# Optimization experiments

Measured on AMD Instinct MI355X. Metric: run time of the kernel, lower is better.

The kernel has to match this reference:

```python
import jax, jax.numpy as jnp
import numpy as np

B, S, D, H = 2, 2048, 768, 12
DH = D // H


def setup_inputs() -> dict:
    key = jax.random.key(0)
    ks = jax.random.split(key, 12)
    f32 = jnp.float32
    sd = 1.0 / np.sqrt(D)
    return {
        "q": jax.random.normal(ks[0], (B, S, D), f32),
        "k": jax.random.normal(ks[1], (B, S, D), f32),
        "v": jax.random.normal(ks[2], (B, S, D), f32),
        "mask": jax.random.normal(ks[3], (S, S), f32),
        "Wq": jax.random.normal(ks[4], (D, D), f32) * sd,
        "bq": jnp.zeros((D,), f32),
        "Wk": jax.random.normal(ks[5], (D, D), f32) * sd,
        "bk": jnp.zeros((D,), f32),
        "Wv": jax.random.normal(ks[6], (D, D), f32) * sd,
        "bv": jnp.zeros((D,), f32),
        "Wo": jax.random.normal(ks[7], (D, D), f32) * sd,
        "bo": jnp.zeros((D,), f32),
    }


def reference(q, k, v, mask, Wq, bq, Wk, bk, Wv, bv, Wo, bo):
    # torch nn.Linear: y = x @ W.T + b
    qh = (q @ Wq.T + bq).reshape(B, S, H, DH).transpose(0, 2, 1, 3)  # [B,H,S,DH]
    kh = (k @ Wk.T + bk).reshape(B, S, H, DH).transpose(0, 2, 1, 3)
    vh = (v @ Wv.T + bv).reshape(B, S, H, DH).transpose(0, 2, 1, 3)
    scores = jnp.einsum("bhsd,bhtd->bhst", qh, kh)  # [B,H,S,S]
    # original adds mask after permute to [H,B,S,S]; with an [S,S] mask the
    # broadcast add is identical either way
    scores = scores + mask
    attn = jax.nn.softmax(scores.astype(jnp.float32) / np.sqrt(DH), axis=-1)
    out = jnp.einsum("bhst,bhtd->bhsd", attn, vh)  # [B,H,S,DH]
    out = out.transpose(0, 2, 1, 3).reshape(B, S, D)
    return out @ Wo.T + bo
```

## Files before the change

### kernel.cpp

```cpp
#include <hip/hip_runtime.h>
#include <hip/hip_bf16.h>

#define B_ 2
#define S_ 2048
#define D_ 768
#define H_ 12
#define DH_ 64
#define M_ (B_*S_)
#define BH_ (B_*H_)

typedef __bf16 v8bf __attribute__((ext_vector_type(8)));
typedef __bf16 v4bf __attribute__((ext_vector_type(4)));
typedef float  v4f  __attribute__((ext_vector_type(4)));

static __device__ __forceinline__ v4f mfma16(v8bf a, v8bf b, v4f c) {
  return __builtin_amdgcn_mfma_f32_16x16x32_bf16(a, b, c, 0, 0, 0);
}

static __device__ __forceinline__ void gload_lds16(const __bf16* g, __bf16* l) {
  __builtin_amdgcn_global_load_lds(
      (const __attribute__((address_space(1))) unsigned int*)g,
      (__attribute__((address_space(3))) unsigned int*)l,
      16, 0, 0);
}

#define C1_ 0.18033688011112042f

__global__ __launch_bounds__(256) void convert_kernel(
    const float* __restrict__ q, const float* __restrict__ k, const float* __restrict__ v,
    const float* __restrict__ Wq, const float* __restrict__ Wk,
    const float* __restrict__ Wv, const float* __restrict__ Wo,
    __bf16* __restrict__ Xq, __bf16* __restrict__ Xk, __bf16* __restrict__ Xv,
    __bf16* __restrict__ Wqb, __bf16* __restrict__ Wkb,
    __bf16* __restrict__ Wvb, __bf16* __restrict__ Wob)
{
  const float* src; __bf16* dst; int n;
  switch (blockIdx.y) {
    case 0: src = q;  dst = Xq;  n = M_*D_; break;
    case 1: src = k;  dst = Xk;  n = M_*D_; break;
    case 2: src = v;  dst = Xv;  n = M_*D_; break;
    case 3: src = Wq; dst = Wqb; n = D_*D_; break;
    case 4: src = Wk; dst = Wkb; n = D_*D_; break;
    case 5: src = Wv; dst = Wvb; n = D_*D_; break;
    default: src = Wo; dst = Wob; n = D_*D_; break;
  }
  int n4 = n >> 2;
  for (int i = blockIdx.x*blockDim.x + threadIdx.x; i < n4; i += gridDim.x*blockDim.x) {
    float4 x = ((const float4*)src)[i];
    v4bf y;
    y[0] = (__bf16)x.x; y[1] = (__bf16)x.y; y[2] = (__bf16)x.z; y[3] = (__bf16)x.w;
    ((v4bf*)dst)[i] = y;
  }
}

__global__ __launch_bounds__(256) void em_kernel(
    const float* __restrict__ mask, __bf16* __restrict__ em)
{
  int t = blockIdx.x*256 + threadIdx.x;
  int L = t & 63; int rest = t >> 6;
  int w = rest & 7; rest >>= 3;
  int kt = rest & 63; rest >>= 6;
  int qt = rest;
  int row = qt*128 + w*16 + (L & 15);
  int key0 = kt*32 + ((L >> 4) << 2);
  const float* mp = mask + (size_t)row*S_ + key0;
  float4 m0 = *(const float4*)mp;
  float4 m1 = *(const float4*)(mp + 16);
  v8bf e;
  e[0] = (__bf16)exp2f(C1_*m0.x); e[1] = (__bf16)exp2f(C1_*m0.y);
  e[2] = (__bf16)exp2f(C1_*m0.z); e[3] = (__bf16)exp2f(C1_*m0.w);
  e[4] = (__bf16)exp2f(C1_*m1.x); e[5] = (__bf16)exp2f(C1_*m1.y);
  e[6] = (__bf16)exp2f(C1_*m1.z); e[7] = (__bf16)exp2f(C1_*m1.w);
  *(v8bf*)(em + (size_t)t*8) = e;
}

static __device__ __forceinline__ void gemm128_pipe(
    const __bf16* __restrict__ A, const __bf16* __restrict__ W,
    int m0, int n0, __bf16* lds, v4f acc[4][4])
{
  const int lane = threadIdx.x & 63;
  const int wave = threadIdx.x >> 6;
  const int r16 = lane & 15;
  const int kc8 = (lane >> 4) << 3;
  const int ia = (wave >> 1) << 2;
  const int ib = (wave & 1) << 2;

  const __bf16* gsrc[4]; int ldo[4];
  #pragma unroll
  for (int t = 0; t < 4; t++) {
    int fb = wave*4 + t;
    gsrc[t] = (fb < 8)
        ? A + (size_t)(m0 + fb*16 + r16)*D_ + kc8
        : W + (size_t)(n0 + (fb - 8)*16 + r16)*D_ + kc8;
    ldo[t] = fb << 9;
  }

  asm volatile("" ::: "memory");
  #pragma unroll
  for (int t = 0; t < 4; t++) gload_lds16(gsrc[t], lds + ldo[t]);
  asm volatile("" ::: "memory");
  #pragma unroll
  for (int t = 0; t < 4; t++) gload_lds16(gsrc[t] + 32, lds + 8192 + ldo[t]);
  asm volatile("" ::: "memory");

#define G_STEP(CUR, NXTB, KC, ISSUE, WSTR) { \
    asm volatile("s_waitcnt vmcnt(" WSTR ")" ::: "memory"); \
    __builtin_amdgcn_s_barrier(); \
    asm volatile("" ::: "memory"); \
    if (ISSUE) { \
      _Pragma("unroll") \
      for (int t = 0; t < 4; t++) \
        gload_lds16(gsrc[t] + (KC), lds + (NXTB)*8192 + ldo[t]); \
    } \
    const __bf16* buf = lds + (CUR)*8192; \
    v8bf a[4], b[4]; \
    _Pragma("unroll") \
    for (int i = 0; i < 4; i++) a[i] = *(const v8bf*)(buf + ((ia+i) << 9) + lane*8); \
    _Pragma("unroll") \
    for (int j = 0; j < 4; j++) b[j] = *(const v8bf*)(buf + ((8+ib+j) << 9) + lane*8); \
    _Pragma("unroll") \
    for (int i = 0; i < 4; i++) \
      _Pragma("unroll") \
      for (int j = 0; j < 4; j++) \
        acc[i][j] = mfma16(a[i], b[j], acc[i][j]); \
  }

  #pragma unroll 1
  for (int ks0 = 0; ks0 < 18; ks0 += 3) {
    G_STEP(0, 2, (ks0+2)*32, true, "4");
    G_STEP(1, 0, (ks0+3)*32, true, "4");
    G_STEP(2, 1, (ks0+4)*32, true, "4");
  }
  G_STEP(0, 2, 20*32, true,  "4");
  G_STEP(1, 0, 21*32, true,  "4");
  G_STEP(2, 1, 22*32, true,  "4");
  G_STEP(0, 2, 23*32, true,  "4");
  G_STEP(1, 0, 0,     false, "4");
  G_STEP(2, 0, 0,     false, "0");
#undef G_STEP
}

__global__ __launch_bounds__(256, 3) void qkv_gemm(
    const __bf16* __restrict__ Xq, const __bf16* __restrict__ Xk, const __bf16* __restrict__ Xv,
    const __bf16* __restrict__ Wqb, const __bf16* __restrict__ Wkb, const __bf16* __restrict__ Wvb,
    const float* __restrict__ bq, const float* __restrict__ bk, const float* __restrict__ bv,
    __bf16* __restrict__ qf, __bf16* __restrict__ kf, __bf16* __restrict__ vf)
{
  __shared__ __bf16 lds[3*8192];
  const int mode = blockIdx.z;
  const __bf16* A = (mode == 0) ? Xq : (mode == 1) ? Xk : Xv;
  const __bf16* W = (mode == 0) ? Wqb : (mode == 1) ? Wkb : Wvb;
  const float* bias = (mode == 0) ? bq : (mode == 1) ? bk : bv;
  const int m0 = blockIdx.y << 7, n0 = blockIdx.x << 7;
  v4f acc[4][4];
  #pragma unroll
  for (int i = 0; i < 4; i++)
    #pragma unroll
    for (int j = 0; j < 4; j++) { v4f z = {0.f,0.f,0.f,0.f}; acc[i][j] = z; }
  gemm128_pipe(A, W, m0, n0, lds, acc);

  const int lane = threadIdx.x & 63;
  const int wave = threadIdx.x >> 6;
  const int wm = (wave >> 1) << 6, wn = (wave & 1) << 6;
  const int col = lane & 15, quad = lane >> 4;
  float bb[4]; int nn[4];
  #pragma unroll
  for (int j = 0; j < 4; j++) { nn[j] = n0 + wn + 16*j + col; bb[j] = bias[nn[j]]; }

  if (mode < 2) {
    __bf16* dst = (mode == 0) ? qf : kf;
    const float sc = (mode == 0) ? C1_ : 1.0f;
    #pragma unroll
    for (int i = 0; i < 4; i++)
      #pragma unroll
      for (int r = 0; r < 4; r++) {
        int m = m0 + wm + 16*i + quad*4 + r;
        int batch = m >> 11, s = m & (S_-1);
        #pragma unroll
        for (int j = 0; j < 4; j++) {
          int n = nn[j];
          int h = n >> 6, dd = n & 63;
          size_t flat = (((size_t)(batch*H_ + h)*128 + (s >> 4))*2 + (dd >> 5))*512
                      + ((((dd >> 3) & 3)*16 + (s & 15)) << 3) + (dd & 7);
          dst[flat] = (__bf16)((acc[i][j][r] + bb[j]) * sc);
        }
      }
  } else {
    #pragma unroll
    for (int i = 0; i < 4; i++) {
      int mbase = m0 + wm + 16*i + quad*4;
      int batch = mbase >> 11, s0 = mbase & (S_-1);
      #pragma unroll
      for (int j = 0; j < 4; j++) {
        int n = nn[j];
        int h = n >> 6, dd = n & 63;
        v4bf pk;
        #pragma unroll
        for (int r = 0; r < 4; r++) pk[r] = (__bf16)(acc[i][j][r] + bb[j]);
        size_t flat = (((size_t)(batch*H_ + h)*64 + (s0 >> 5))*4 + (dd >> 4))*512
                    + ((((s0 >> 3) & 3)*16 + (dd & 15)) << 3) + (s0 & 7);
        *(v4bf*)(vf + flat) = pk;
      }
    }
  }
}

__global__ __launch_bounds__(512, 2) void attn_kernel(
    const __bf16* __restrict__ qf, const __bf16* __restrict__ kf, const __bf16* __restrict__ vf,
    const __bf16* __restrict__ em, __bf16* __restrict__ ao)
{
  __shared__ __bf16 kv[4][2][2048];
  __shared__ __bf16 plds[8][16][40];

  const int bh = blockIdx.y;
  const int qt = blockIdx.x;
  const int wave = threadIdx.x >> 6, lane = threadIdx.x & 63;
  const int col = lane & 15, quad = lane >> 4, koff = quad << 3;
  const int batch = bh / H_, h = bh % H_;
  const __bf16* qfb = qf + (size_t)bh * (S_*DH_);
  const __bf16* kfb = kf + (size_t)bh * (S_*DH_);
  const __bf16* vfb = vf + (size_t)bh * (S_*DH_);
  const __bf16* emw = em + (size_t)qt * 262144 + wave*512 + lane*8;
  __bf16 (*pt)[40] = plds[wave];

  const __bf16* gsrc = ((wave < 4) ? kfb : vfb) + ((wave & 3) << 9) + lane*8;
  __bf16* kvd[4];
  #pragma unroll
  for (int b = 0; b < 4; b++) kvd[b] = &kv[b][wave >> 2][(wave & 3) << 9];

  const __bf16* qblk = qfb + (size_t)(qt*8 + wave)*1024;
  v8bf Qf0 = *(const v8bf*)(qblk + lane*8);
  v8bf Qf1 = *(const v8bf*)(qblk + 512 + lane*8);

  v4f O[4];
  #pragma unroll
  for (int f = 0; f < 4; f++) { v4f z = {0.f,0.f,0.f,0.f}; O[f] = z; }
  float li = 0.f;

  asm volatile("" ::: "memory");
  gload_lds16(gsrc, kvd[0]);
  v8bf ef0 = *(const v8bf*)(emw);
  asm volatile("" ::: "memory");
  gload_lds16(gsrc + 2048, kvd[1]);
  v8bf ef1 = *(const v8bf*)(emw + 4096);
  v8bf ef2, ef3;

#define ATT_STEP(P, EFC, EFN, ISSUE, WSTR) \
  { \
    asm volatile("s_waitcnt vmcnt(" WSTR ")" ::: "memory"); \
    __builtin_amdgcn_s_barrier(); \
    asm volatile("" ::: "memory"); \
    if (ISSUE) { \
      const int nkt = kt0 + (P) + 2; \
      gload_lds16(gsrc + (size_t)nkt*2048, kvd[((P)+2)&3]); \
      EFN = *(const v8bf*)(emw + (size_t)nkt*4096); \
    } \
    const __bf16* Kb = kv[(P)&3][0]; \
    const __bf16* Vb = kv[(P)&3][1]; \
    v8bf Ka0 = *(const v8bf*)(Kb + lane*8); \
    v8bf Ka1 = *(const v8bf*)(Kb + 512 + lane*8); \
    v8bf Ka2 = *(const v8bf*)(Kb + 1024 + lane*8); \
    v8bf Ka3 = *(const v8bf*)(Kb + 1536 + lane*8); \
    v4f s0 = {0.f,0.f,0.f,0.f}, s1 = {0.f,0.f,0.f,0.f}; \
    s0 = mfma16(Ka0, Qf0, s0); s0 = mfma16(Ka1, Qf1, s0); \
    s1 = mfma16(Ka2, Qf0, s1); s1 = mfma16(Ka3, Qf1, s1); \
    float p[8], rs = 0.f; \
    _Pragma("unroll") \
    for (int j = 0; j < 4; j++) { \
      p[j]   = exp2f(s0[j]) * (float)EFC[j]; \
      p[4+j] = exp2f(s1[j]) * (float)EFC[4+j]; \
    } \
    _Pragma("unroll") \
    for (int j = 0; j < 8; j++) rs += p[j]; \
    li += rs; \
    v4bf pk0, pk1; \
    _Pragma("unroll") \
    for (int r = 0; r < 4; r++) { pk0[r] = (__bf16)p[r]; pk1[r] = (__bf16)p[4+r]; } \
    *(v4bf*)(&pt[col][quad*4])      = pk0; \
    *(v4bf*)(&pt[col][16 + quad*4]) = pk1; \
    v8bf Pf = *(const v8bf*)(&pt[col][koff]); \
    v8bf Vf0 = *(const v8bf*)(Vb + lane*8); \
    v8bf Vf1 = *(const v8bf*)(Vb + 512 + lane*8); \
    v8bf Vf2 = *(const v8bf*)(Vb + 1024 + lane*8); \
    v8bf Vf3 = *(const v8bf*)(Vb + 1536 + lane*8); \
    O[0] = mfma16(Vf0, Pf, O[0]); \
    O[1] = mfma16(Vf1, Pf, O[1]); \
    O[2] = mfma16(Vf2, Pf, O[2]); \
    O[3] = mfma16(Vf3, Pf, O[3]); \
  }

  #pragma unroll 1
  for (int kt0 = 0; kt0 < 60; kt0 += 4) {
    ATT_STEP(0, ef0, ef2, true, "2");
    ATT_STEP(1, ef1, ef3, true, "2");
    ATT_STEP(2, ef2, ef0, true, "2");
    ATT_STEP(3, ef3, ef1, true, "2");
  }
  {
    const int kt0 = 60;
    ATT_STEP(0, ef0, ef2, true,  "2");
    ATT_STEP(1, ef1, ef3, true,  "2");
    ATT_STEP(2, ef2, ef0, false, "2");
    ATT_STEP(3, ef3, ef1, false, "0");
  }
#undef ATT_STEP

  float rs = li;
  rs += __shfl_xor(rs, 16);
  rs += __shfl_xor(rs, 32);
  float invl = 1.f / rs;
  const int qg = (qt << 7) + (wave << 4) + col;
  __bf16* orow = ao + ((size_t)batch*S_ + qg)*D_ + h*DH_ + quad*4;
  #pragma unroll
  for (int f = 0; f < 4; f++) {
    v4bf o;
    #pragma unroll
    for (int r = 0; r < 4; r++) o[r] = (__bf16)(O[f][r] * invl);
    *(v4bf*)(orow + f*16) = o;
  }
}

__global__ __launch_bounds__(256, 3) void out_gemm(
    const __bf16* __restrict__ Ao, const __bf16* __restrict__ Wob,
    const float* __restrict__ bo, float* __restrict__ out)
{
  __shared__ __bf16 lds[3*8192];
  const int m0 = blockIdx.y << 7, n0 = blockIdx.x << 7;
  v4f acc[4][4];
  #pragma unroll
  for (int i = 0; i < 4; i++)
    #pragma unroll
    for (int j = 0; j < 4; j++) { v4f z = {0.f,0.f,0.f,0.f}; acc[i][j] = z; }
  gemm128_pipe(Ao, Wob, m0, n0, lds, acc);

  const int lane = threadIdx.x & 63;
  const int wave = threadIdx.x >> 6;
  const int wm = (wave >> 1) << 6, wn = (wave & 1) << 6;
  const int col = lane & 15, quad = lane >> 4;
  float bb[4]; int nn[4];
  #pragma unroll
  for (int j = 0; j < 4; j++) { nn[j] = n0 + wn + 16*j + col; bb[j] = bo[nn[j]]; }
  #pragma unroll
  for (int i = 0; i < 4; i++)
    #pragma unroll
    for (int r = 0; r < 4; r++) {
      int m = m0 + wm + 16*i + quad*4 + r;
      #pragma unroll
      for (int j = 0; j < 4; j++)
        out[(size_t)m*D_ + nn[j]] = acc[i][j][r] + bb[j];
    }
}

extern "C" void kernel_launch(void* const* d_in, const int* in_sizes, int n_in,
                              void* d_out, int out_size, void* d_ws, size_t ws_size,
                              hipStream_t stream)
{
  const float* q    = (const float*)d_in[0];
  const float* k    = (const float*)d_in[1];
  const float* v    = (const float*)d_in[2];
  const float* mask = (const float*)d_in[3];
  const float* Wq   = (const float*)d_in[4];
  const float* bq   = (const float*)d_in[5];
  const float* Wk   = (const float*)d_in[6];
  const float* bk   = (const float*)d_in[7];
  const float* Wv   = (const float*)d_in[8];
  const float* bv   = (const float*)d_in[9];
  const float* Wo   = (const float*)d_in[10];
  const float* bo   = (const float*)d_in[11];

  const size_t XN = (size_t)M_ * D_;
  const size_t WN = (size_t)D_ * D_;
  const size_t HN = (size_t)BH_ * S_ * DH_;

  char* ws = (char*)d_ws;
  __bf16* Xq  = (__bf16*)ws;                 ws += XN * 2;
  __bf16* Xk  = (__bf16*)ws;                 ws += XN * 2;
  __bf16* Xv  = (__bf16*)ws;                 ws += XN * 2;
  __bf16* Wqb = (__bf16*)ws;                 ws += WN * 2;
  __bf16* Wkb = (__bf16*)ws;                 ws += WN * 2;
  __bf16* Wvb = (__bf16*)ws;                 ws += WN * 2;
  __bf16* Wob = (__bf16*)ws;                 ws += WN * 2;
  __bf16* qfb = (__bf16*)ws;                 ws += HN * 2;
  __bf16* kfb = (__bf16*)ws;                 ws += HN * 2;
  __bf16* vfb = (__bf16*)ws;                 ws += HN * 2;
  __bf16* aob = (__bf16*)ws;                 ws += XN * 2;
  __bf16* emb = Xq;

  convert_kernel<<<dim3(768, 7), 256, 0, stream>>>(
      q, k, v, Wq, Wk, Wv, Wo, Xq, Xk, Xv, Wqb, Wkb, Wvb, Wob);
  qkv_gemm<<<dim3(6, 32, 3), 256, 0, stream>>>(
      Xq, Xk, Xv, Wqb, Wkb, Wvb, bq, bk, bv, qfb, kfb, vfb);
  em_kernel<<<dim3(2048), 256, 0, stream>>>(mask, emb);
  attn_kernel<<<dim3(16, 24), 512, 0, stream>>>(qfb, kfb, vfb, emb, aob);
  out_gemm<<<dim3(6, 32), 256, 0, stream>>>(aob, Wob, bo, (float*)d_out);
}
```

Before: 239.5 us.

## Switch attention to 32x32x16 MFMA with register-shuffled P and 4-wave blocks

Rewrites the attention kernel to use 32x32x16 bf16 MFMA tiles, so each wave handles 32 query rows instead of 16, and blocks shrink to 4 waves. The Q/K/V fragment layouts written by the QKV GEMM and the exp(mask) layout are changed to match. The P matrix now moves from accumulator layout to operand layout through cross-lane shuffles instead of an LDS round trip, which removes per-step LDS stores and loads. Each wave now loads both K and V slices, so there are more in-flight loads per wave, fewer waves per block, and more register pressure.

```diff
diff --git a/kernel.cpp b/kernel.cpp
--- a/kernel.cpp
+++ b/kernel.cpp
@@ -12,9 +12,13 @@
 typedef __bf16 v8bf __attribute__((ext_vector_type(8)));
 typedef __bf16 v4bf __attribute__((ext_vector_type(4)));
 typedef float  v4f  __attribute__((ext_vector_type(4)));
+typedef float  f32x16 __attribute__((ext_vector_type(16)));
 
 static __device__ __forceinline__ v4f mfma16(v8bf a, v8bf b, v4f c) {
   return __builtin_amdgcn_mfma_f32_16x16x32_bf16(a, b, c, 0, 0, 0);
+}
+static __device__ __forceinline__ f32x16 mfma32(v8bf a, v8bf b, f32x16 c) {
+  return __builtin_amdgcn_mfma_f32_32x32x16_bf16(a, b, c, 0, 0, 0);
 }
 
 static __device__ __forceinline__ void gload_lds16(const __bf16* g, __bf16* l) {
@@ -58,20 +62,27 @@
 {
   int t = blockIdx.x*256 + threadIdx.x;
   int L = t & 63; int rest = t >> 6;
-  int w = rest & 7; rest >>= 3;
+  int w = rest & 3; rest >>= 2;
   int kt = rest & 63; rest >>= 6;
   int qt = rest;
-  int row = qt*128 + w*16 + (L & 15);
-  int key0 = kt*32 + ((L >> 4) << 2);
+  int row = qt*128 + w*32 + (L & 31);
+  int key0 = kt*32 + ((L >> 5) << 2);
   const float* mp = mask + (size_t)row*S_ + key0;
-  float4 m0 = *(const float4*)mp;
-  float4 m1 = *(const float4*)(mp + 16);
-  v8bf e;
-  e[0] = (__bf16)exp2f(C1_*m0.x); e[1] = (__bf16)exp2f(C1_*m0.y);
-  e[2] = (__bf16)exp2f(C1_*m0.z); e[3] = (__bf16)exp2f(C1_*m0.w);
-  e[4] = (__bf16)exp2f(C1_*m1.x); e[5] = (__bf16)exp2f(C1_*m1.y);
-  e[6] = (__bf16)exp2f(C1_*m1.z); e[7] = (__bf16)exp2f(C1_*m1.w);
-  *(v8bf*)(em + (size_t)t*8) = e;
+  float4 m0 = *(const float4*)(mp);
+  float4 m1 = *(const float4*)(mp + 8);
+  float4 m2 = *(const float4*)(mp + 16);
+  float4 m3 = *(const float4*)(mp + 24);
+  v8bf e0, e1;
+  e0[0] = (__bf16)exp2f(C1_*m0.x); e0[1] = (__bf16)exp2f(C1_*m0.y);
+  e0[2] = (__bf16)exp2f(C1_*m0.z); e0[3] = (__bf16)exp2f(C1_*m0.w);
+  e0[4] = (__bf16)exp2f(C1_*m1.x); e0[5] = (__bf16)exp2f(C1_*m1.y);
+  e0[6] = (__bf16)exp2f(C1_*m1.z); e0[7] = (__bf16)exp2f(C1_*m1.w);
+  e1[0] = (__bf16)exp2f(C1_*m2.x); e1[1] = (__bf16)exp2f(C1_*m2.y);
+  e1[2] = (__bf16)exp2f(C1_*m2.z); e1[3] = (__bf16)exp2f(C1_*m2.w);
+  e1[4] = (__bf16)exp2f(C1_*m3.x); e1[5] = (__bf16)exp2f(C1_*m3.y);
+  e1[6] = (__bf16)exp2f(C1_*m3.z); e1[7] = (__bf16)exp2f(C1_*m3.w);
+  *(v8bf*)(em + (size_t)t*16)     = e0;
+  *(v8bf*)(em + (size_t)t*16 + 8) = e1;
 }
 
 static __device__ __forceinline__ void gemm128_pipe(
@@ -176,12 +187,13 @@
       for (int r = 0; r < 4; r++) {
         int m = m0 + wm + 16*i + quad*4 + r;
         int batch = m >> 11, s = m & (S_-1);
+        int q32 = s >> 5, s31 = s & 31;
         #pragma unroll
         for (int j = 0; j < 4; j++) {
           int n = nn[j];
           int h = n >> 6, dd = n & 63;
-          size_t flat = (((size_t)(batch*H_ + h)*128 + (s >> 4))*2 + (dd >> 5))*512
-                      + ((((dd >> 3) & 3)*16 + (s & 15)) << 3) + (dd & 7);
+          size_t flat = (((size_t)(batch*H_ + h)*64 + q32)*4 + (dd >> 4))*512
+                      + ((((dd >> 3) & 1)*32 + s31) << 3) + (dd & 7);
           dst[flat] = (__bf16)((acc[i][j][r] + bb[j]) * sc);
         }
       }
@@ -197,126 +209,152 @@
         v4bf pk;
         #pragma unroll
         for (int r = 0; r < 4; r++) pk[r] = (__bf16)(acc[i][j][r] + bb[j]);
-        size_t flat = (((size_t)(batch*H_ + h)*64 + (s0 >> 5))*4 + (dd >> 4))*512
-                    + ((((s0 >> 3) & 3)*16 + (dd & 15)) << 3) + (s0 & 7);
+        size_t flat = ((((size_t)(batch*H_ + h)*64 + (s0 >> 5))*2 + (dd >> 5))*2 + ((s0 >> 4) & 1))*512
+                    + ((((s0 >> 3) & 1)*32 + (dd & 31)) << 3) + (s0 & 7);
         *(v4bf*)(vf + flat) = pk;
       }
     }
   }
 }
 
-__global__ __launch_bounds__(512, 2) void attn_kernel(
+__global__ __launch_bounds__(256, 2) void attn_kernel(
     const __bf16* __restrict__ qf, const __bf16* __restrict__ kf, const __bf16* __restrict__ vf,
     const __bf16* __restrict__ em, __bf16* __restrict__ ao)
 {
   __shared__ __bf16 kv[4][2][2048];
-  __shared__ __bf16 plds[8][16][40];
 
   const int bh = blockIdx.y;
   const int qt = blockIdx.x;
   const int wave = threadIdx.x >> 6, lane = threadIdx.x & 63;
-  const int col = lane & 15, quad = lane >> 4, koff = quad << 3;
+  const int q5 = lane & 31, hi = lane >> 5;
   const int batch = bh / H_, h = bh % H_;
   const __bf16* qfb = qf + (size_t)bh * (S_*DH_);
   const __bf16* kfb = kf + (size_t)bh * (S_*DH_);
   const __bf16* vfb = vf + (size_t)bh * (S_*DH_);
-  const __bf16* emw = em + (size_t)qt * 262144 + wave*512 + lane*8;
-  __bf16 (*pt)[40] = plds[wave];
-
-  const __bf16* gsrc = ((wave < 4) ? kfb : vfb) + ((wave & 3) << 9) + lane*8;
-  __bf16* kvd[4];
-  #pragma unroll
-  for (int b = 0; b < 4; b++) kvd[b] = &kv[b][wave >> 2][(wave & 3) << 9];
-
-  const __bf16* qblk = qfb + (size_t)(qt*8 + wave)*1024;
-  v8bf Qf0 = *(const v8bf*)(qblk + lane*8);
-  v8bf Qf1 = *(const v8bf*)(qblk + 512 + lane*8);
-
-  v4f O[4];
-  #pragma unroll
-  for (int f = 0; f < 4; f++) { v4f z = {0.f,0.f,0.f,0.f}; O[f] = z; }
+  const __bf16* emw = em + (size_t)qt*262144 + wave*1024 + lane*16;
+
+  const int q32 = qt*4 + wave;
+  v8bf Qb[4];
+  #pragma unroll
+  for (int s4 = 0; s4 < 4; s4++)
+    Qb[s4] = *(const v8bf*)(qfb + ((size_t)q32*4 + s4)*512 + lane*8);
+
+  const __bf16* gK = kfb + wave*512 + lane*8;
+  const __bf16* gV = vfb + wave*512 + lane*8;
+  __bf16* kd[4]; __bf16* vd[4];
+  #pragma unroll
+  for (int b = 0; b < 4; b++) { kd[b] = &kv[b][0][wave*512]; vd[b] = &kv[b][1][wave*512]; }
+
+  f32x16 O0, O1;
+  #pragma unroll
+  for (int z = 0; z < 16; z++) { O0[z] = 0.f; O1[z] = 0.f; }
   float li = 0.f;
 
   asm volatile("" ::: "memory");
-  gload_lds16(gsrc, kvd[0]);
-  v8bf ef0 = *(const v8bf*)(emw);
+  gload_lds16(gK, kd[0]);
+  gload_lds16(gV, vd[0]);
+  v8bf e0a = *(const v8bf*)(emw);
+  v8bf e0b = *(const v8bf*)(emw + 8);
   asm volatile("" ::: "memory");
-  gload_lds16(gsrc + 2048, kvd[1]);
-  v8bf ef1 = *(const v8bf*)(emw + 4096);
-  v8bf ef2, ef3;
-
-#define ATT_STEP(P, EFC, EFN, ISSUE, WSTR) \
+  gload_lds16(gK + 2048, kd[1]);
+  gload_lds16(gV + 2048, vd[1]);
+  v8bf e1a = *(const v8bf*)(emw + 4096);
+  v8bf e1b = *(const v8bf*)(emw + 4104);
+  v8bf e2a, e2b, e3a, e3b;
+
+#define ATT_STEP(P, EA, EB, NA, NB, ISSUE, WSTR) \
   { \
     asm volatile("s_waitcnt vmcnt(" WSTR ")" ::: "memory"); \
     __builtin_amdgcn_s_barrier(); \
     asm volatile("" ::: "memory"); \
     if (ISSUE) { \
       const int nkt = kt0 + (P) + 2; \
-      gload_lds16(gsrc + (size_t)nkt*2048, kvd[((P)+2)&3]); \
-      EFN = *(const v8bf*)(emw + (size_t)nkt*4096); \
+      gload_lds16(gK + (size_t)nkt*2048, kd[((P)+2)&3]); \
+      gload_lds16(gV + (size_t)nkt*2048, vd[((P)+2)&3]); \
+      NA = *(const v8bf*)(emw + (size_t)nkt*4096); \
+      NB = *(const v8bf*)(emw + (size_t)nkt*4096 + 8); \
     } \
     const __bf16* Kb = kv[(P)&3][0]; \
     const __bf16* Vb = kv[(P)&3][1]; \
-    v8bf Ka0 = *(const v8bf*)(Kb + lane*8); \
-    v8bf Ka1 = *(const v8bf*)(Kb + 512 + lane*8); \
-    v8bf Ka2 = *(const v8bf*)(Kb + 1024 + lane*8); \
-    v8bf Ka3 = *(const v8bf*)(Kb + 1536 + lane*8); \
-    v4f s0 = {0.f,0.f,0.f,0.f}, s1 = {0.f,0.f,0.f,0.f}; \
-    s0 = mfma16(Ka0, Qf0, s0); s0 = mfma16(Ka1, Qf1, s0); \
-    s1 = mfma16(Ka2, Qf0, s1); s1 = mfma16(Ka3, Qf1, s1); \
-    float p[8], rs = 0.f; \
-    _Pragma("unroll") \
-    for (int j = 0; j < 4; j++) { \
-      p[j]   = exp2f(s0[j]) * (float)EFC[j]; \
-      p[4+j] = exp2f(s1[j]) * (float)EFC[4+j]; \
+    f32x16 Sx; \
+    _Pragma("unroll") \
+    for (int z = 0; z < 16; z++) Sx[z] = 0.f; \
+    _Pragma("unroll") \
+    for (int s4 = 0; s4 < 4; s4++) { \
+      v8bf Ka = *(const v8bf*)(Kb + s4*512 + lane*8); \
+      Sx = mfma32(Ka, Qb[s4], Sx); \
     } \
-    _Pragma("unroll") \
-    for (int j = 0; j < 8; j++) rs += p[j]; \
+    float p[16]; float rs = 0.f; \
+    _Pragma("unroll") \
+    for (int r = 0; r < 8; r++) p[r] = exp2f(Sx[r]) * (float)EA[r]; \
+    _Pragma("unroll") \
+    for (int r = 0; r < 8; r++) p[8+r] = exp2f(Sx[8+r]) * (float)EB[r]; \
+    _Pragma("unroll") \
+    for (int r = 0; r < 16; r++) rs += p[r]; \
     li += rs; \
-    v4bf pk0, pk1; \
-    _Pragma("unroll") \
-    for (int r = 0; r < 4; r++) { pk0[r] = (__bf16)p[r]; pk1[r] = (__bf16)p[4+r]; } \
-    *(v4bf*)(&pt[col][quad*4])      = pk0; \
-    *(v4bf*)(&pt[col][16 + quad*4]) = pk1; \
-    v8bf Pf = *(const v8bf*)(&pt[col][koff]); \
-    v8bf Vf0 = *(const v8bf*)(Vb + lane*8); \
-    v8bf Vf1 = *(const v8bf*)(Vb + 512 + lane*8); \
-    v8bf Vf2 = *(const v8bf*)(Vb + 1024 + lane*8); \
-    v8bf Vf3 = *(const v8bf*)(Vb + 1536 + lane*8); \
-    O[0] = mfma16(Vf0, Pf, O[0]); \
-    O[1] = mfma16(Vf1, Pf, O[1]); \
-    O[2] = mfma16(Vf2, Pf, O[2]); \
-    O[3] = mfma16(Vf3, Pf, O[3]); \
+    unsigned g0,g1,g2,g3,g4,g5,g6,g7; \
+    { union { __bf16 hh[2]; unsigned u; } t_; \
+      t_.hh[0]=(__bf16)p[0];  t_.hh[1]=(__bf16)p[1];  g0=t_.u; \
+      t_.hh[0]=(__bf16)p[2];  t_.hh[1]=(__bf16)p[3];  g1=t_.u; \
+      t_.hh[0]=(__bf16)p[4];  t_.hh[1]=(__bf16)p[5];  g2=t_.u; \
+      t_.hh[0]=(__bf16)p[6];  t_.hh[1]=(__bf16)p[7];  g3=t_.u; \
+      t_.hh[0]=(__bf16)p[8];  t_.hh[1]=(__bf16)p[9];  g4=t_.u; \
+      t_.hh[0]=(__bf16)p[10]; t_.hh[1]=(__bf16)p[11]; g5=t_.u; \
+      t_.hh[0]=(__bf16)p[12]; t_.hh[1]=(__bf16)p[13]; g6=t_.u; \
+      t_.hh[0]=(__bf16)p[14]; t_.hh[1]=(__bf16)p[15]; g7=t_.u; } \
+    unsigned x0 = __shfl_xor(g0, 32), x1 = __shfl_xor(g1, 32); \
+    unsigned x2 = __shfl_xor(g2, 32), x3 = __shfl_xor(g3, 32); \
+    unsigned x4 = __shfl_xor(g4, 32), x5 = __shfl_xor(g5, 32); \
+    unsigned x6 = __shfl_xor(g6, 32), x7 = __shfl_xor(g7, 32); \
+    union { unsigned u[4]; v8bf v; } bp0, bp1; \
+    bp0.u[0] = hi ? x2 : g0;    \
+    bp0.u[1] = hi ? x3 : g1;    \
+    bp0.u[2] = hi ? g2 : x0;    \
+    bp0.u[3] = hi ? g3 : x1;    \
+    bp1.u[0] = hi ? x6 : g4; \
+    bp1.u[1] = hi ? x7 : g5; \
+    bp1.u[2] = hi ? g6 : x4; \
+    bp1.u[3] = hi ? g7 : x5; \
+    v8bf Va00 = *(const v8bf*)(Vb + lane*8); \
+    v8bf Va01 = *(const v8bf*)(Vb + 512 + lane*8); \
+    v8bf Va10 = *(const v8bf*)(Vb + 1024 + lane*8); \
+    v8bf Va11 = *(const v8bf*)(Vb + 1536 + lane*8); \
+    O0 = mfma32(Va00, bp0.v, O0); \
+    O0 = mfma32(Va01, bp1.v, O0); \
+    O1 = mfma32(Va10, bp0.v, O1); \
+    O1 = mfma32(Va11, bp1.v, O1); \
   }
 
   #pragma unroll 1
   for (int kt0 = 0; kt0 < 60; kt0 += 4) {
-    ATT_STEP(0, ef0, ef2, true, "2");
-    ATT_STEP(1, ef1, ef3, true, "2");
-    ATT_STEP(2, ef2, ef0, true, "2");
-    ATT_STEP(3, ef3, ef1, true, "2");
+    ATT_STEP(0, e0a, e0b, e2a, e2b, true, "4");
+    ATT_STEP(1, e1a, e1b, e3a, e3b, true, "4");
+    ATT_STEP(2, e2a, e2b, e0a, e0b, true, "4");
+    ATT_STEP(3, e3a, e3b, e1a, e1b, true, "4");
   }
   {
     const int kt0 = 60;
-    ATT_STEP(0, ef0, ef2, true,  "2");
-    ATT_STEP(1, ef1, ef3, true,  "2");
-    ATT_STEP(2, ef2, ef0, false, "2");
-    ATT_STEP(3, ef3, ef1, false, "0");
+    ATT_STEP(0, e0a, e0b, e2a, e2b, true,  "4");
+    ATT_STEP(1, e1a, e1b, e3a, e3b, true,  "4");
+    ATT_STEP(2, e2a, e2b, e0a, e0b, false, "4");
+    ATT_STEP(3, e3a, e3b, e1a, e1b, false, "0");
   }
 #undef ATT_STEP
 
-  float rs = li;
-  rs += __shfl_xor(rs, 16);
-  rs += __shfl_xor(rs, 32);
-  float invl = 1.f / rs;
-  const int qg = (qt << 7) + (wave << 4) + col;
-  __bf16* orow = ao + ((size_t)batch*S_ + qg)*D_ + h*DH_ + quad*4;
-  #pragma unroll
-  for (int f = 0; f < 4; f++) {
-    v4bf o;
-    #pragma unroll
-    for (int r = 0; r < 4; r++) o[r] = (__bf16)(O[f][r] * invl);
-    *(v4bf*)(orow + f*16) = o;
+  li += __shfl_xor(li, 32);
+  float invl = 1.f / li;
+  const int qg = qt*128 + wave*32 + q5;
+  __bf16* orow = ao + ((size_t)batch*S_ + qg)*D_ + h*DH_;
+  #pragma unroll
+  for (int g = 0; g < 4; g++) {
+    v4bf o0, o1;
+    #pragma unroll
+    for (int r = 0; r < 4; r++) {
+      o0[r] = (__bf16)(O0[g*4+r] * invl);
+      o1[r] = (__bf16)(O1[g*4+r] * invl);
+    }
+    *(v4bf*)(orow + g*8 + hi*4)      = o0;
+    *(v4bf*)(orow + 32 + g*8 + hi*4) = o1;
   }
 }
 
@@ -390,7 +428,7 @@
       q, k, v, Wq, Wk, Wv, Wo, Xq, Xk, Xv, Wqb, Wkb, Wvb, Wob);
   qkv_gemm<<<dim3(6, 32, 3), 256, 0, stream>>>(
       Xq, Xk, Xv, Wqb, Wkb, Wvb, bq, bk, bv, qfb, kfb, vfb);
-  em_kernel<<<dim3(2048), 256, 0, stream>>>(mask, emb);
-  attn_kernel<<<dim3(16, 24), 512, 0, stream>>>(qfb, kfb, vfb, emb, aob);
+  em_kernel<<<dim3(1024), 256, 0, stream>>>(mask, emb);
+  attn_kernel<<<dim3(16, 24), 256, 0, stream>>>(qfb, kfb, vfb, emb, aob);
   out_gemm<<<dim3(6, 32), 256, 0, stream>>>(aob, Wob, bo, (float*)d_out);
 }
```

After: 248.1 us. 3.6% more time.

## Fuse fp32-to-bf16 conversion into QKV GEMM loads and merge Wo conversion into mask kernel

Applied to the files above, without the earlier changes.

The standalone convert kernel is removed. The QKV GEMM now reads fp32 activations and weights straight from global memory into registers, converts them to bf16, and writes them to a double-buffered LDS tile, with register prefetch two steps ahead. The Wo conversion moves into extra blocks of the mask-exponent kernel, which now writes to its own workspace region instead of reusing the converted-input buffer. This drops one launch and the bf16 intermediate round-trip through global memory. In exchange, the GEMM moves twice the bytes per tile, gives up direct global-to-LDS loads for register staging, and drops from three LDS buffers to two with a lower occupancy hint.

```diff
diff --git a/kernel.cpp b/kernel.cpp
--- a/kernel.cpp
+++ b/kernel.cpp
@@ -26,37 +26,20 @@
 
 #define C1_ 0.18033688011112042f
 
-__global__ __launch_bounds__(256) void convert_kernel(
-    const float* __restrict__ q, const float* __restrict__ k, const float* __restrict__ v,
-    const float* __restrict__ Wq, const float* __restrict__ Wk,
-    const float* __restrict__ Wv, const float* __restrict__ Wo,
-    __bf16* __restrict__ Xq, __bf16* __restrict__ Xk, __bf16* __restrict__ Xv,
-    __bf16* __restrict__ Wqb, __bf16* __restrict__ Wkb,
-    __bf16* __restrict__ Wvb, __bf16* __restrict__ Wob)
-{
-  const float* src; __bf16* dst; int n;
-  switch (blockIdx.y) {
-    case 0: src = q;  dst = Xq;  n = M_*D_; break;
-    case 1: src = k;  dst = Xk;  n = M_*D_; break;
-    case 2: src = v;  dst = Xv;  n = M_*D_; break;
-    case 3: src = Wq; dst = Wqb; n = D_*D_; break;
-    case 4: src = Wk; dst = Wkb; n = D_*D_; break;
-    case 5: src = Wv; dst = Wvb; n = D_*D_; break;
-    default: src = Wo; dst = Wob; n = D_*D_; break;
-  }
-  int n4 = n >> 2;
-  for (int i = blockIdx.x*blockDim.x + threadIdx.x; i < n4; i += gridDim.x*blockDim.x) {
-    float4 x = ((const float4*)src)[i];
+__global__ __launch_bounds__(256) void em_kernel(
+    const float* __restrict__ mask, const float* __restrict__ Wo,
+    __bf16* __restrict__ em, __bf16* __restrict__ Wob)
+{
+  int bx = blockIdx.x;
+  if (bx >= 2048) {
+    int i = (bx - 2048)*256 + threadIdx.x;
+    float4 x = ((const float4*)Wo)[i];
     v4bf y;
     y[0] = (__bf16)x.x; y[1] = (__bf16)x.y; y[2] = (__bf16)x.z; y[3] = (__bf16)x.w;
-    ((v4bf*)dst)[i] = y;
-  }
-}
-
-__global__ __launch_bounds__(256) void em_kernel(
-    const float* __restrict__ mask, __bf16* __restrict__ em)
-{
-  int t = blockIdx.x*256 + threadIdx.x;
+    ((v4bf*)Wob)[i] = y;
+    return;
+  }
+  int t = bx*256 + threadIdx.x;
   int L = t & 63; int rest = t >> 6;
   int w = rest & 7; rest >>= 3;
   int kt = rest & 63; rest >>= 6;
@@ -74,6 +57,100 @@
   *(v8bf*)(em + (size_t)t*8) = e;
 }
 
+static __device__ __forceinline__ void gemm128_cvt(
+    const float* __restrict__ A, const float* __restrict__ W,
+    int m0, int n0, __bf16* lds, v4f acc[4][4])
+{
+  const int lane = threadIdx.x & 63;
+  const int wave = threadIdx.x >> 6;
+  const int r16 = lane & 15;
+  const int kc8 = (lane >> 4) << 3;
+  const int ia = (wave >> 1) << 2;
+  const int ib = (wave & 1) << 2;
+
+  const float* gsrc[4]; int ldo[4];
+  #pragma unroll
+  for (int t = 0; t < 4; t++) {
+    int fb = wave*4 + t;
+    gsrc[t] = (fb < 8)
+        ? A + (size_t)(m0 + fb*16 + r16)*D_ + kc8
+        : W + (size_t)(n0 + (fb - 8)*16 + r16)*D_ + kc8;
+    ldo[t] = (fb << 9) + lane*8;
+  }
+
+  float4 rbA[4][2], rbB[4][2];
+
+  asm volatile("" ::: "memory");
+  #pragma unroll
+  for (int t = 0; t < 4; t++) {
+    rbA[t][0] = *(const float4*)(gsrc[t]);
+    rbA[t][1] = *(const float4*)(gsrc[t] + 4);
+  }
+  asm volatile("" ::: "memory");
+  #pragma unroll
+  for (int t = 0; t < 4; t++) {
+    rbB[t][0] = *(const float4*)(gsrc[t] + 32);
+    rbB[t][1] = *(const float4*)(gsrc[t] + 36);
+  }
+  asm volatile("" ::: "memory");
+  asm volatile("s_waitcnt vmcnt(8)" ::: "memory");
+  #pragma unroll
+  for (int t = 0; t < 4; t++) {
+    v8bf w8;
+    w8[0]=(__bf16)rbA[t][0].x; w8[1]=(__bf16)rbA[t][0].y;
+    w8[2]=(__bf16)rbA[t][0].z; w8[3]=(__bf16)rbA[t][0].w;
+    w8[4]=(__bf16)rbA[t][1].x; w8[5]=(__bf16)rbA[t][1].y;
+    w8[6]=(__bf16)rbA[t][1].z; w8[7]=(__bf16)rbA[t][1].w;
+    *(v8bf*)(lds + ldo[t]) = w8;
+  }
+  asm volatile("s_waitcnt lgkmcnt(0)" ::: "memory");
+  __builtin_amdgcn_s_barrier();
+
+#define Q_STEP(CUR, RI, RW, KC2, ISSUE, DOWRITE, WSTR) { \
+    if (ISSUE) { \
+      _Pragma("unroll") \
+      for (int t = 0; t < 4; t++) { \
+        RI[t][0] = *(const float4*)(gsrc[t] + (KC2)); \
+        RI[t][1] = *(const float4*)(gsrc[t] + (KC2) + 4); \
+      } \
+    } \
+    asm volatile("s_waitcnt vmcnt(" WSTR ")" ::: "memory"); \
+    if (DOWRITE) { \
+      _Pragma("unroll") \
+      for (int t = 0; t < 4; t++) { \
+        v8bf w8; \
+        w8[0]=(__bf16)RW[t][0].x; w8[1]=(__bf16)RW[t][0].y; \
+        w8[2]=(__bf16)RW[t][0].z; w8[3]=(__bf16)RW[t][0].w; \
+        w8[4]=(__bf16)RW[t][1].x; w8[5]=(__bf16)RW[t][1].y; \
+        w8[6]=(__bf16)RW[t][1].z; w8[7]=(__bf16)RW[t][1].w; \
+        *(v8bf*)(lds + ((CUR)^1)*8192 + ldo[t]) = w8; \
+      } \
+    } \
+    const __bf16* buf = lds + (CUR)*8192; \
+    v8bf a[4], b[4]; \
+    _Pragma("unroll") \
+    for (int i = 0; i < 4; i++) a[i] = *(const v8bf*)(buf + ((ia+i) << 9) + lane*8); \
+    _Pragma("unroll") \
+    for (int j = 0; j < 4; j++) b[j] = *(const v8bf*)(buf + ((8+ib+j) << 9) + lane*8); \
+    _Pragma("unroll") \
+    for (int i = 0; i < 4; i++) \
+      _Pragma("unroll") \
+      for (int j = 0; j < 4; j++) \
+        acc[i][j] = mfma16(a[i], b[j], acc[i][j]); \
+    asm volatile("s_waitcnt lgkmcnt(0)" ::: "memory"); \
+    __builtin_amdgcn_s_barrier(); \
+  }
+
+  #pragma unroll 1
+  for (int ks0 = 0; ks0 < 22; ks0 += 2) {
+    Q_STEP(0, rbA, rbB, (ks0+2)*32, true, true, "8");
+    Q_STEP(1, rbB, rbA, (ks0+3)*32, true, true, "8");
+  }
+  Q_STEP(0, rbA, rbB, 0, false, true,  "0");
+  Q_STEP(1, rbB, rbA, 0, false, false, "0");
+#undef Q_STEP
+}
+
 static __device__ __forceinline__ void gemm128_pipe(
     const __bf16* __restrict__ A, const __bf16* __restrict__ W,
     int m0, int n0, __bf16* lds, v4f acc[4][4])
@@ -140,16 +217,16 @@
 #undef G_STEP
 }
 
-__global__ __launch_bounds__(256, 3) void qkv_gemm(
-    const __bf16* __restrict__ Xq, const __bf16* __restrict__ Xk, const __bf16* __restrict__ Xv,
-    const __bf16* __restrict__ Wqb, const __bf16* __restrict__ Wkb, const __bf16* __restrict__ Wvb,
+__global__ __launch_bounds__(256, 2) void qkv_gemm(
+    const float* __restrict__ Xq, const float* __restrict__ Xk, const float* __restrict__ Xv,
+    const float* __restrict__ Wq, const float* __restrict__ Wk, const float* __restrict__ Wv,
     const float* __restrict__ bq, const float* __restrict__ bk, const float* __restrict__ bv,
     __bf16* __restrict__ qf, __bf16* __restrict__ kf, __bf16* __restrict__ vf)
 {
-  __shared__ __bf16 lds[3*8192];
+  __shared__ __bf16 lds[2*8192];
   const int mode = blockIdx.z;
-  const __bf16* A = (mode == 0) ? Xq : (mode == 1) ? Xk : Xv;
-  const __bf16* W = (mode == 0) ? Wqb : (mode == 1) ? Wkb : Wvb;
+  const float* A = (mode == 0) ? Xq : (mode == 1) ? Xk : Xv;
+  const float* W = (mode == 0) ? Wq : (mode == 1) ? Wk : Wv;
   const float* bias = (mode == 0) ? bq : (mode == 1) ? bk : bv;
   const int m0 = blockIdx.y << 7, n0 = blockIdx.x << 7;
   v4f acc[4][4];
@@ -157,7 +234,7 @@
   for (int i = 0; i < 4; i++)
     #pragma unroll
     for (int j = 0; j < 4; j++) { v4f z = {0.f,0.f,0.f,0.f}; acc[i][j] = z; }
-  gemm128_pipe(A, W, m0, n0, lds, acc);
+  gemm128_cvt(A, W, m0, n0, lds, acc);
 
   const int lane = threadIdx.x & 63;
   const int wave = threadIdx.x >> 6;
@@ -371,26 +448,19 @@
   const size_t XN = (size_t)M_ * D_;
   const size_t WN = (size_t)D_ * D_;
   const size_t HN = (size_t)BH_ * S_ * DH_;
+  const size_t EN = (size_t)524288 * 8;
 
   char* ws = (char*)d_ws;
-  __bf16* Xq  = (__bf16*)ws;                 ws += XN * 2;
-  __bf16* Xk  = (__bf16*)ws;                 ws += XN * 2;
-  __bf16* Xv  = (__bf16*)ws;                 ws += XN * 2;
-  __bf16* Wqb = (__bf16*)ws;                 ws += WN * 2;
-  __bf16* Wkb = (__bf16*)ws;                 ws += WN * 2;
-  __bf16* Wvb = (__bf16*)ws;                 ws += WN * 2;
   __bf16* Wob = (__bf16*)ws;                 ws += WN * 2;
   __bf16* qfb = (__bf16*)ws;                 ws += HN * 2;
   __bf16* kfb = (__bf16*)ws;                 ws += HN * 2;
   __bf16* vfb = (__bf16*)ws;                 ws += HN * 2;
   __bf16* aob = (__bf16*)ws;                 ws += XN * 2;
-  __bf16* emb = Xq;
-
-  convert_kernel<<<dim3(768, 7), 256, 0, stream>>>(
-      q, k, v, Wq, Wk, Wv, Wo, Xq, Xk, Xv, Wqb, Wkb, Wvb, Wob);
+  __bf16* emb = (__bf16*)ws;                 ws += EN * 2;
+
+  em_kernel<<<dim3(2624), 256, 0, stream>>>(mask, Wo, emb, Wob);
   qkv_gemm<<<dim3(6, 32, 3), 256, 0, stream>>>(
-      Xq, Xk, Xv, Wqb, Wkb, Wvb, bq, bk, bv, qfb, kfb, vfb);
-  em_kernel<<<dim3(2048), 256, 0, stream>>>(mask, emb);
+      q, k, v, Wq, Wk, Wv, bq, bk, bv, qfb, kfb, vfb);
   attn_kernel<<<dim3(16, 24), 512, 0, stream>>>(qfb, kfb, vfb, emb, aob);
   out_gemm<<<dim3(6, 32), 256, 0, stream>>>(aob, Wob, bo, (float*)d_out);
 }
```

New measurement: 257.8 us. +7.6%, slower.
